# Kernel tuning notes

Measured on AMD Instinct MI355X. Metric: run time of the kernel, lower is better.

Reference implementation:

```python
import jax
import jax.numpy as jnp
from jax import lax
import numpy as np

VOCAB = 50000
EMB = 32
HID = 32
LAYERS = 4
BATCH = 8192
SEQ = 111


def setup_inputs() -> dict:
    key = jax.random.key(0)
    ks = jax.random.split(key, 12)
    s = 0.1
    x = jax.random.randint(ks[0], (BATCH, SEQ), 0, VOCAB, dtype=jnp.int64 if jax.config.read('jax_enable_x64') else jnp.int32)
    emb = jax.random.normal(ks[1], (VOCAB, EMB), jnp.float32) * s
    # stacked per-layer LSTM weights; layer-0 input dim == EMB == HID so stacking is valid
    Wih = jax.random.normal(ks[2], (LAYERS, 4 * HID, EMB), jnp.float32) * s
    Whh = jax.random.normal(ks[3], (LAYERS, 4 * HID, HID), jnp.float32) * s
    bih = jax.random.normal(ks[4], (LAYERS, 4 * HID), jnp.float32) * s
    bhh = jax.random.normal(ks[5], (LAYERS, 4 * HID), jnp.float32) * s
    Wa = jax.random.normal(ks[6], (HID, 1), jnp.float32) * s
    ba = jax.random.normal(ks[7], (1,), jnp.float32) * s
    W1 = jax.random.normal(ks[8], (HID, 32), jnp.float32) * s
    b1 = jax.random.normal(ks[9], (32,), jnp.float32) * s
    W2 = jax.random.normal(ks[10], (32, 3), jnp.float32) * s
    b2 = jax.random.normal(ks[11], (3,), jnp.float32) * s
    return {"x": x, "emb": emb, "Wih": Wih, "Whh": Whh, "bih": bih, "bhh": bhh,
            "Wa": Wa, "ba": ba, "W1": W1, "b1": b1, "W2": W2, "b2": b2}


def _lstm_layer(x, Wih, Whh, bih, bhh):
    # x: [B, T, D] -> [B, T, H]; PyTorch gate order: i, f, g, o
    B = x.shape[0]
    H = Whh.shape[1]
    # precompute the input contribution for all timesteps (one big GEMM)
    xg = jnp.einsum('btd,gd->btg', x, Wih) + bih + bhh  # [B, T, 4H]

    def step(carry, xg_t):
        h, c = carry
        z = xg_t + h @ Whh.T  # [B, 4H]
        i, f, g, o = jnp.split(z, 4, axis=-1)
        c = jax.nn.sigmoid(f) * c + jax.nn.sigmoid(i) * jnp.tanh(g)
        h = jax.nn.sigmoid(o) * jnp.tanh(c)
        return (h, c), h

    init = (jnp.zeros((B, H), x.dtype), jnp.zeros((B, H), x.dtype))
    _, hs = lax.scan(step, init, jnp.swapaxes(xg, 0, 1))  # hs: [T, B, H]
    return jnp.swapaxes(hs, 0, 1)


def reference(x, emb, Wih, Whh, bih, bhh, Wa, ba, W1, b1, W2, b2):
    h = emb[x]  # [B, T, E]
    for l in range(Wih.shape[0]):  # fixed 4 layers
        h = _lstm_layer(h, Wih[l], Whh[l], bih[l], bhh[l])
    scores = h @ Wa + ba                       # [B, T, 1]
    attn = jax.nn.softmax(scores, axis=1)      # softmax over time
    context = jnp.sum(h * attn, axis=1)        # [B, H]
    hid = jnp.tanh(context @ W1 + b1)          # dropout is identity at eval
    return hid @ W2 + b2                       # [B, 3]
```

## Files before the change

### kernel.cpp

```cpp
#include <hip/hip_runtime.h>

#define TSEQ 111
#define L2E 1.44269504088896340736f
#define TWO_L2E 2.88539008177792680472f

using f32x4  = __attribute__((ext_vector_type(4))) float;
using f32x2  = __attribute__((ext_vector_type(2))) float;
using short8 = __attribute__((ext_vector_type(8))) short;

union FragU { unsigned u[4]; uint4 v; short8 s; };

__device__ __forceinline__ float fexp2(float x) { return __builtin_amdgcn_exp2f(x); }
__device__ __forceinline__ float frcp(float x)  { return __builtin_amdgcn_rcpf(x); }
__device__ __forceinline__ float tanh2(float zs) { return 1.f - 2.f * frcp(1.f + fexp2(zs + zs)); }
__device__ __forceinline__ f32x2 exp2v(f32x2 x) { f32x2 r; r[0] = fexp2(x[0]); r[1] = fexp2(x[1]); return r; }
__device__ __forceinline__ f32x2 rcpv(f32x2 x)  { f32x2 r; r[0] = frcp(x[0]); r[1] = frcp(x[1]); return r; }

__device__ __forceinline__ unsigned rnd_bf16(float w) {
  unsigned u = __float_as_uint(w);
  return (u + 0x7fffu + ((u >> 16) & 1u)) >> 16;
}
__device__ __forceinline__ unsigned cvtpk(float a, float b) {
  unsigned r;
  asm("v_cvt_pk_bf16_f32 %0, %1, %2" : "=v"(r) : "v"(a), "v"(b));
  return r;
}

__global__ __launch_bounds__(512, 4) void lstm_fused(
    const int* __restrict__ x, const float* __restrict__ emb,
    const float* __restrict__ Wih, const float* __restrict__ Whh,
    const float* __restrict__ bih, const float* __restrict__ bhh,
    const float* __restrict__ Wa, const float* __restrict__ W1,
    const float* __restrict__ b1, const float* __restrict__ W2,
    const float* __restrict__ b2, float* __restrict__ out)
{
  __shared__ __align__(16) unsigned short hb[2 * 4 * 512];

  const int tid  = threadIdx.x;
  const int wvu  = __builtin_amdgcn_readfirstlane(tid) >> 6;
  const int l    = wvu >> 1;
  const int hf   = wvu & 1;
  const int lane = tid & 63;
  const int c    = lane & 15;
  const int q    = lane >> 4;
  const int gcc  = (c & 3) ^ (c >> 2);
  const int rowbase = blockIdx.x * 16;
  const int xrow = (rowbase + c) * TSEQ;

  const int rdOff = c * 32 + ((q ^ gcc) << 3);
  const int wrOff = c * 32 + ((((2 * hf + (q >> 1)) ^ gcc) << 3) | ((q & 1) << 2));

  FragU wihf[4], whhf[4];
#pragma unroll
  for (int g = 0; g < 4; ++g) {
    const float sj = (g == 2) ? TWO_L2E : -L2E;
    const int wr = 32 * g + 16 * hf + c;
    const float* srcI = Wih + l * 4096 + wr * 32 + 8 * q;
    const float* srcH = Whh + l * 4096 + wr * 32 + 8 * q;
#pragma unroll
    for (int p = 0; p < 4; ++p) {
      wihf[g].u[p] = rnd_bf16(srcI[2 * p] * sj) | (rnd_bf16(srcI[2 * p + 1] * sj) << 16);
      whhf[g].u[p] = rnd_bf16(srcH[2 * p] * sj) | (rnd_bf16(srcH[2 * p + 1] * sj) << 16);
    }
  }
  f32x4 bvv[4];
#pragma unroll
  for (int g = 0; g < 4; ++g) {
    const float sj = (g == 2) ? TWO_L2E : -L2E;
    const int bi = l * 128 + 32 * g + 16 * hf + 4 * q;
#pragma unroll
    for (int e = 0; e < 4; ++e)
      bvv[g][e] = (bih[bi + e] + bhh[bi + e]) * sj;
  }

  FragU wahA, walA;
#pragma unroll
  for (int p = 0; p < 4; ++p) { wahA.u[p] = 0u; walA.u[p] = 0u; }
  if (l == 3) {
#pragma unroll
    for (int p = 0; p < 4; ++p) {
      const int k0 = 8 * q + 2 * p;
      float w0 = Wa[k0] * L2E, w1 = Wa[k0 + 1] * L2E;
      unsigned h0 = rnd_bf16(w0), h1b = rnd_bf16(w1);
      wahA.u[p] = h0 | (h1b << 16);
      float l0v = w0 - __uint_as_float(h0 << 16);
      float l1v = w1 - __uint_as_float(h1b << 16);
      walA.u[p] = rnd_bf16(l0v) | (rnd_bf16(l1v) << 16);
    }
  }

  f32x2 cs2[2];
  cs2[0] = (f32x2){0.f, 0.f}; cs2[1] = (f32x2){0.f, 0.f};
  float mr = -1e30f, sr = 0.f, cx[4];
#pragma unroll
  for (int e = 0; e < 4; ++e) cx[e] = 0.f;

  for (int i = tid; i < 2 * 4 * 512 / 2; i += 512) ((unsigned*)hb)[i] = 0u;

  float4 emA = make_float4(0.f, 0.f, 0.f, 0.f), emB = emA;
  int idxn = 0;
  if (l == 0) {
    int i0 = x[xrow];
    emA = *(const float4*)(emb + i0 * 32 + 8 * q);
    emB = *(const float4*)(emb + i0 * 32 + 8 * q + 4);
    idxn = x[xrow + 1];
  }
  __syncthreads();

#pragma unroll 2
  for (int s = 0; s < TSEQ + 4; ++s) {
    const int t = s - l;
    const bool active = ((unsigned)t < (unsigned)TSEQ);
    const int rp = (s + 1) & 1;
    const int wp = s & 1;
    const bool doAtt = (l == 3) && (s >= 4);

    FragU fi, fh;
    __builtin_amdgcn_s_setprio(1);
    if (active) {
      if (l == 0) {
        fi.u[0] = cvtpk(emA.x, emA.y); fi.u[1] = cvtpk(emA.z, emA.w);
        fi.u[2] = cvtpk(emB.x, emB.y); fi.u[3] = cvtpk(emB.z, emB.w);
        if (t + 1 < TSEQ) {
          emA = *(const float4*)(emb + idxn * 32 + 8 * q);
          emB = *(const float4*)(emb + idxn * 32 + 8 * q + 4);
        }
        if (t + 2 < TSEQ) idxn = x[xrow + t + 2];
      } else {
        fi.v = *(const uint4*)(hb + (rp * 4 + (l - 1)) * 512 + rdOff);
      }
    }
    if (active || doAtt)
      fh.v = *(const uint4*)(hb + (rp * 4 + l) * 512 + rdOff);

    f32x4 acc[4];
    if (active) {
#pragma unroll
      for (int g = 0; g < 4; ++g) {
        acc[g] = __builtin_amdgcn_mfma_f32_16x16x32_bf16(wihf[g].s, fi.s, bvv[g], 0, 0, 0);
        acc[g] = __builtin_amdgcn_mfma_f32_16x16x32_bf16(whhf[g].s, fh.s, acc[g], 0, 0, 0);
      }
    }
    f32x4 sacc;
    if (doAtt) {
      f32x4 z = {0.f, 0.f, 0.f, 0.f};
      sacc = __builtin_amdgcn_mfma_f32_16x16x32_bf16(wahA.s, fh.s, z, 0, 0, 0);
      sacc = __builtin_amdgcn_mfma_f32_16x16x32_bf16(walA.s, fh.s, sacc, 0, 0, 0);
    }
    __builtin_amdgcn_s_setprio(0);

    if (active) {
      float hv[4];
      const f32x2 one = {1.f, 1.f};
      const f32x2 tl2 = {TWO_L2E, TWO_L2E};
#pragma unroll
      for (int pr2 = 0; pr2 < 2; ++pr2) {
        const int e0 = 2 * pr2;
        f32x2 va; va[0] = acc[0][e0]; va[1] = acc[0][e0 + 1];
        f32x2 vm; vm[0] = acc[1][e0]; vm[1] = acc[1][e0 + 1];
        f32x2 vb; vb[0] = acc[2][e0]; vb[1] = acc[2][e0 + 1];
        f32x2 vp; vp[0] = acc[3][e0]; vp[1] = acc[3][e0 + 1];
        f32x2 ea = exp2v(va), em_ = exp2v(vm), eb = exp2v(vb), ep = exp2v(vp);
        f32x2 P  = (one + ea) * (one + eb);
        f32x2 M1 = one + em_;
        f32x2 num = cs2[pr2] * P + (eb - one) * M1;
        f32x2 cn = num * rcpv(M1 * P);
        cs2[pr2] = cn;
        f32x2 qa = cn * tl2;
        qa[0] = fminf(qa[0], 80.f); qa[1] = fminf(qa[1], 80.f);
        f32x2 qv = exp2v(qa);
        f32x2 hvv = (qv - one) * rcpv((one + ep) * (one + qv));
        hv[e0] = hvv[0]; hv[e0 + 1] = hvv[1];
      }

      *(uint2*)(hb + (wp * 4 + l) * 512 + wrOff) =
          make_uint2(cvtpk(hv[0], hv[1]), cvtpk(hv[2], hv[3]));
    }

    if (doAtt) {
      float pf = sacc[0];
      float mn = fmaxf(mr, pf);
      float sc = fexp2(mr - mn);
      float pr = fexp2(pf - mn);
      sr = sr * sc + pr;
#pragma unroll
      for (int p = 0; p < 2; ++p) {
        unsigned w = fh.u[2 * hf + p];
        float vlo = __uint_as_float(w << 16);
        float vhi = __uint_as_float(w & 0xffff0000u);
        cx[2 * p]     = cx[2 * p]     * sc + pr * vlo;
        cx[2 * p + 1] = cx[2 * p + 1] * sc + pr * vhi;
      }
      mr = mn;
    }

    asm volatile("s_waitcnt lgkmcnt(0)\n\ts_barrier" ::: "memory");
  }

  __syncthreads();

  float* cb = (float*)hb;
  if (l == 3) {
    float inv = frcp(sr);
#pragma unroll
    for (int e = 0; e < 4; ++e)
      cb[c * 33 + 8 * q + 4 * hf + e] = cx[e] * inv;
  }
  __syncthreads();
  if (wvu != 6) return;

  float a0[4], a1[4];
  {
    float bb0 = b1[c], bb1 = b1[c + 16];
#pragma unroll
    for (int e = 0; e < 4; ++e) { a0[e] = bb0; a1[e] = bb1; }
    for (int j = 0; j < 32; ++j) {
      float w0 = W1[j * 32 + c];
      float w1 = W1[j * 32 + c + 16];
#pragma unroll
      for (int e = 0; e < 4; ++e) {
        float cr = cb[(4 * q + e) * 33 + j];
        a0[e] = fmaf(cr, w0, a0[e]);
        a1[e] = fmaf(cr, w1, a1[e]);
      }
    }
  }
  float o0[4], o1[4], o2[4];
  {
    float w20 = W2[c * 3 + 0], w21 = W2[c * 3 + 1], w22 = W2[c * 3 + 2];
    float w30 = W2[(c + 16) * 3 + 0], w31 = W2[(c + 16) * 3 + 1], w32 = W2[(c + 16) * 3 + 2];
#pragma unroll
    for (int e = 0; e < 4; ++e) {
      float h0 = tanh2(a0[e] * L2E);
      float hB = tanh2(a1[e] * L2E);
      o0[e] = h0 * w20 + hB * w30;
      o1[e] = h0 * w21 + hB * w31;
      o2[e] = h0 * w22 + hB * w32;
    }
  }
#pragma unroll
  for (int mk = 1; mk <= 8; mk <<= 1) {
#pragma unroll
    for (int e = 0; e < 4; ++e) {
      o0[e] += __shfl_xor(o0[e], mk, 64);
      o1[e] += __shfl_xor(o1[e], mk, 64);
      o2[e] += __shfl_xor(o2[e], mk, 64);
    }
  }
  if (c < 3) {
    float bb = b2[c];
#pragma unroll
    for (int e = 0; e < 4; ++e) {
      float v = (c == 0) ? o0[e] : ((c == 1) ? o1[e] : o2[e]);
      out[(rowbase + 4 * q + e) * 3 + c] = v + bb;
    }
  }
}

extern "C" void kernel_launch(void* const* d_in, const int* in_sizes, int n_in,
                              void* d_out, int out_size, void* d_ws, size_t ws_size,
                              hipStream_t stream) {
  const int*   x   = (const int*)d_in[0];
  const float* emb = (const float*)d_in[1];
  const float* Wih = (const float*)d_in[2];
  const float* Whh = (const float*)d_in[3];
  const float* bih = (const float*)d_in[4];
  const float* bhh = (const float*)d_in[5];
  const float* Wa  = (const float*)d_in[6];
  const float* W1  = (const float*)d_in[8];
  const float* b1  = (const float*)d_in[9];
  const float* W2  = (const float*)d_in[10];
  const float* b2  = (const float*)d_in[11];
  float* out = (float*)d_out;

  lstm_fused<<<512, 512, 0, stream>>>(x, emb, Wih, Whh, bih, bhh, Wa, W1, b1, W2, b2, out);
}
```

Baseline: 159.8 us.

## Process two 16-row batch tiles per block to interleave independent recurrences

Each block now handles 32 batch rows as two independent 16-row tiles, so every wave issues two sets of MFMAs and gate computations per timestep. The grid is halved and shared memory doubled to hold both tiles' hidden states. The intent is to give each wave independent work to hide MFMA and transcendental latency along the serial recurrence and to amortize the per-step barrier. The cost is higher register pressure (launch bounds relaxed to 2) and fewer blocks overall.

```diff
diff --git a/kernel.cpp b/kernel.cpp
--- a/kernel.cpp
+++ b/kernel.cpp
@@ -26,7 +26,31 @@
   return r;
 }
 
-__global__ __launch_bounds__(512, 4) void lstm_fused(
+__device__ __forceinline__ void gates(const f32x4 acc[4], f32x2 cs2[2], float hv[4]) {
+  const f32x2 one = {1.f, 1.f};
+  const f32x2 tl2 = {TWO_L2E, TWO_L2E};
+#pragma unroll
+  for (int pr2 = 0; pr2 < 2; ++pr2) {
+    const int e0 = 2 * pr2;
+    f32x2 va; va[0] = acc[0][e0]; va[1] = acc[0][e0 + 1];
+    f32x2 vm; vm[0] = acc[1][e0]; vm[1] = acc[1][e0 + 1];
+    f32x2 vb; vb[0] = acc[2][e0]; vb[1] = acc[2][e0 + 1];
+    f32x2 vp; vp[0] = acc[3][e0]; vp[1] = acc[3][e0 + 1];
+    f32x2 ea = exp2v(va), em_ = exp2v(vm), eb = exp2v(vb), ep = exp2v(vp);
+    f32x2 P  = (one + ea) * (one + eb);
+    f32x2 M1 = one + em_;
+    f32x2 num = cs2[pr2] * P + (eb - one) * M1;
+    f32x2 cn = num * rcpv(M1 * P);
+    cs2[pr2] = cn;
+    f32x2 qa = cn * tl2;
+    qa[0] = fminf(qa[0], 80.f); qa[1] = fminf(qa[1], 80.f);
+    f32x2 qv = exp2v(qa);
+    f32x2 hvv = (qv - one) * rcpv((one + ep) * (one + qv));
+    hv[e0] = hvv[0]; hv[e0 + 1] = hvv[1];
+  }
+}
+
+__global__ __launch_bounds__(512, 2) void lstm_fused(
     const int* __restrict__ x, const float* __restrict__ emb,
     const float* __restrict__ Wih, const float* __restrict__ Whh,
     const float* __restrict__ bih, const float* __restrict__ bhh,
@@ -34,7 +58,7 @@
     const float* __restrict__ b1, const float* __restrict__ W2,
     const float* __restrict__ b2, float* __restrict__ out)
 {
-  __shared__ __align__(16) unsigned short hb[2 * 4 * 512];
+  __shared__ __align__(16) unsigned short hb[2 * 4 * 1024];
 
   const int tid  = threadIdx.x;
   const int wvu  = __builtin_amdgcn_readfirstlane(tid) >> 6;
@@ -44,8 +68,9 @@
   const int c    = lane & 15;
   const int q    = lane >> 4;
   const int gcc  = (c & 3) ^ (c >> 2);
-  const int rowbase = blockIdx.x * 16;
-  const int xrow = (rowbase + c) * TSEQ;
+  const int rowbase = blockIdx.x * 32;
+  const int xrow0 = (rowbase + c) * TSEQ;
+  const int xrow1 = (rowbase + 16 + c) * TSEQ;
 
   const int rdOff = c * 32 + ((q ^ gcc) << 3);
   const int wrOff = c * 32 + ((((2 * hf + (q >> 1)) ^ gcc) << 3) | ((q & 1) << 2));
@@ -89,21 +114,27 @@
     }
   }
 
-  f32x2 cs2[2];
-  cs2[0] = (f32x2){0.f, 0.f}; cs2[1] = (f32x2){0.f, 0.f};
-  float mr = -1e30f, sr = 0.f, cx[4];
-#pragma unroll
-  for (int e = 0; e < 4; ++e) cx[e] = 0.f;
-
-  for (int i = tid; i < 2 * 4 * 512 / 2; i += 512) ((unsigned*)hb)[i] = 0u;
-
-  float4 emA = make_float4(0.f, 0.f, 0.f, 0.f), emB = emA;
-  int idxn = 0;
+  f32x2 csA[2], csB[2];
+  csA[0] = (f32x2){0.f, 0.f}; csA[1] = (f32x2){0.f, 0.f};
+  csB[0] = (f32x2){0.f, 0.f}; csB[1] = (f32x2){0.f, 0.f};
+  float mr0 = -1e30f, sr0 = 0.f, cx0[4];
+  float mr1 = -1e30f, sr1 = 0.f, cx1[4];
+#pragma unroll
+  for (int e = 0; e < 4; ++e) { cx0[e] = 0.f; cx1[e] = 0.f; }
+
+  for (int i = tid; i < 2 * 4 * 1024 / 2; i += 512) ((unsigned*)hb)[i] = 0u;
+
+  float4 emA0 = make_float4(0.f, 0.f, 0.f, 0.f), emB0 = emA0, emA1 = emA0, emB1 = emA0;
+  int idxn0 = 0, idxn1 = 0;
   if (l == 0) {
-    int i0 = x[xrow];
-    emA = *(const float4*)(emb + i0 * 32 + 8 * q);
-    emB = *(const float4*)(emb + i0 * 32 + 8 * q + 4);
-    idxn = x[xrow + 1];
+    int i00 = x[xrow0];
+    emA0 = *(const float4*)(emb + i00 * 32 + 8 * q);
+    emB0 = *(const float4*)(emb + i00 * 32 + 8 * q + 4);
+    int i01 = x[xrow1];
+    emA1 = *(const float4*)(emb + i01 * 32 + 8 * q);
+    emB1 = *(const float4*)(emb + i01 * 32 + 8 * q + 4);
+    idxn0 = x[xrow0 + 1];
+    idxn1 = x[xrow1 + 1];
   }
   __syncthreads();
 
@@ -115,83 +146,93 @@
     const int wp = s & 1;
     const bool doAtt = (l == 3) && (s >= 4);
 
-    FragU fi, fh;
+    FragU fi0, fh0, fi1, fh1;
     __builtin_amdgcn_s_setprio(1);
     if (active) {
       if (l == 0) {
-        fi.u[0] = cvtpk(emA.x, emA.y); fi.u[1] = cvtpk(emA.z, emA.w);
-        fi.u[2] = cvtpk(emB.x, emB.y); fi.u[3] = cvtpk(emB.z, emB.w);
+        fi0.u[0] = cvtpk(emA0.x, emA0.y); fi0.u[1] = cvtpk(emA0.z, emA0.w);
+        fi0.u[2] = cvtpk(emB0.x, emB0.y); fi0.u[3] = cvtpk(emB0.z, emB0.w);
+        fi1.u[0] = cvtpk(emA1.x, emA1.y); fi1.u[1] = cvtpk(emA1.z, emA1.w);
+        fi1.u[2] = cvtpk(emB1.x, emB1.y); fi1.u[3] = cvtpk(emB1.z, emB1.w);
         if (t + 1 < TSEQ) {
-          emA = *(const float4*)(emb + idxn * 32 + 8 * q);
-          emB = *(const float4*)(emb + idxn * 32 + 8 * q + 4);
+          emA0 = *(const float4*)(emb + idxn0 * 32 + 8 * q);
+          emB0 = *(const float4*)(emb + idxn0 * 32 + 8 * q + 4);
+          emA1 = *(const float4*)(emb + idxn1 * 32 + 8 * q);
+          emB1 = *(const float4*)(emb + idxn1 * 32 + 8 * q + 4);
         }
-        if (t + 2 < TSEQ) idxn = x[xrow + t + 2];
+        if (t + 2 < TSEQ) { idxn0 = x[xrow0 + t + 2]; idxn1 = x[xrow1 + t + 2]; }
       } else {
-        fi.v = *(const uint4*)(hb + (rp * 4 + (l - 1)) * 512 + rdOff);
-      }
-    }
-    if (active || doAtt)
-      fh.v = *(const uint4*)(hb + (rp * 4 + l) * 512 + rdOff);
-
-    f32x4 acc[4];
+        fi0.v = *(const uint4*)(hb + (rp * 4 + (l - 1)) * 1024 + rdOff);
+        fi1.v = *(const uint4*)(hb + (rp * 4 + (l - 1)) * 1024 + rdOff + 512);
+      }
+    }
+    if (active || doAtt) {
+      fh0.v = *(const uint4*)(hb + (rp * 4 + l) * 1024 + rdOff);
+      fh1.v = *(const uint4*)(hb + (rp * 4 + l) * 1024 + rdOff + 512);
+    }
+
+    f32x4 acc0[4], acc1[4];
     if (active) {
 #pragma unroll
       for (int g = 0; g < 4; ++g) {
-        acc[g] = __builtin_amdgcn_mfma_f32_16x16x32_bf16(wihf[g].s, fi.s, bvv[g], 0, 0, 0);
-        acc[g] = __builtin_amdgcn_mfma_f32_16x16x32_bf16(whhf[g].s, fh.s, acc[g], 0, 0, 0);
-      }
-    }
-    f32x4 sacc;
+        acc0[g] = __builtin_amdgcn_mfma_f32_16x16x32_bf16(wihf[g].s, fi0.s, bvv[g], 0, 0, 0);
+        acc0[g] = __builtin_amdgcn_mfma_f32_16x16x32_bf16(whhf[g].s, fh0.s, acc0[g], 0, 0, 0);
+      }
+#pragma unroll
+      for (int g = 0; g < 4; ++g) {
+        acc1[g] = __builtin_amdgcn_mfma_f32_16x16x32_bf16(wihf[g].s, fi1.s, bvv[g], 0, 0, 0);
+        acc1[g] = __builtin_amdgcn_mfma_f32_16x16x32_bf16(whhf[g].s, fh1.s, acc1[g], 0, 0, 0);
+      }
+    }
+    f32x4 sacc0, sacc1;
     if (doAtt) {
       f32x4 z = {0.f, 0.f, 0.f, 0.f};
-      sacc = __builtin_amdgcn_mfma_f32_16x16x32_bf16(wahA.s, fh.s, z, 0, 0, 0);
-      sacc = __builtin_amdgcn_mfma_f32_16x16x32_bf16(walA.s, fh.s, sacc, 0, 0, 0);
+      sacc0 = __builtin_amdgcn_mfma_f32_16x16x32_bf16(wahA.s, fh0.s, z, 0, 0, 0);
+      sacc0 = __builtin_amdgcn_mfma_f32_16x16x32_bf16(walA.s, fh0.s, sacc0, 0, 0, 0);
+      sacc1 = __builtin_amdgcn_mfma_f32_16x16x32_bf16(wahA.s, fh1.s, z, 0, 0, 0);
+      sacc1 = __builtin_amdgcn_mfma_f32_16x16x32_bf16(walA.s, fh1.s, sacc1, 0, 0, 0);
     }
     __builtin_amdgcn_s_setprio(0);
 
     if (active) {
-      float hv[4];
-      const f32x2 one = {1.f, 1.f};
-      const f32x2 tl2 = {TWO_L2E, TWO_L2E};
-#pragma unroll
-      for (int pr2 = 0; pr2 < 2; ++pr2) {
-        const int e0 = 2 * pr2;
-        f32x2 va; va[0] = acc[0][e0]; va[1] = acc[0][e0 + 1];
-        f32x2 vm; vm[0] = acc[1][e0]; vm[1] = acc[1][e0 + 1];
-        f32x2 vb; vb[0] = acc[2][e0]; vb[1] = acc[2][e0 + 1];
-        f32x2 vp; vp[0] = acc[3][e0]; vp[1] = acc[3][e0 + 1];
-        f32x2 ea = exp2v(va), em_ = exp2v(vm), eb = exp2v(vb), ep = exp2v(vp);
-        f32x2 P  = (one + ea) * (one + eb);
-        f32x2 M1 = one + em_;
-        f32x2 num = cs2[pr2] * P + (eb - one) * M1;
-        f32x2 cn = num * rcpv(M1 * P);
-        cs2[pr2] = cn;
-        f32x2 qa = cn * tl2;
-        qa[0] = fminf(qa[0], 80.f); qa[1] = fminf(qa[1], 80.f);
-        f32x2 qv = exp2v(qa);
-        f32x2 hvv = (qv - one) * rcpv((one + ep) * (one + qv));
-        hv[e0] = hvv[0]; hv[e0 + 1] = hvv[1];
-      }
-
-      *(uint2*)(hb + (wp * 4 + l) * 512 + wrOff) =
-          make_uint2(cvtpk(hv[0], hv[1]), cvtpk(hv[2], hv[3]));
+      float hv0[4], hv1[4];
+      gates(acc0, csA, hv0);
+      *(uint2*)(hb + (wp * 4 + l) * 1024 + wrOff) =
+          make_uint2(cvtpk(hv0[0], hv0[1]), cvtpk(hv0[2], hv0[3]));
+      gates(acc1, csB, hv1);
+      *(uint2*)(hb + (wp * 4 + l) * 1024 + wrOff + 512) =
+          make_uint2(cvtpk(hv1[0], hv1[1]), cvtpk(hv1[2], hv1[3]));
     }
 
     if (doAtt) {
-      float pf = sacc[0];
-      float mn = fmaxf(mr, pf);
-      float sc = fexp2(mr - mn);
-      float pr = fexp2(pf - mn);
-      sr = sr * sc + pr;
-#pragma unroll
-      for (int p = 0; p < 2; ++p) {
-        unsigned w = fh.u[2 * hf + p];
-        float vlo = __uint_as_float(w << 16);
-        float vhi = __uint_as_float(w & 0xffff0000u);
-        cx[2 * p]     = cx[2 * p]     * sc + pr * vlo;
-        cx[2 * p + 1] = cx[2 * p + 1] * sc + pr * vhi;
-      }
-      mr = mn;
+      {
+        float pf = sacc0[0];
+        float mn = fmaxf(mr0, pf);
+        float sc = fexp2(mr0 - mn);
+        float pr = fexp2(pf - mn);
+        sr0 = sr0 * sc + pr;
+#pragma unroll
+        for (int p = 0; p < 2; ++p) {
+          unsigned w = fh0.u[2 * hf + p];
+          cx0[2 * p]     = cx0[2 * p]     * sc + pr * __uint_as_float(w << 16);
+          cx0[2 * p + 1] = cx0[2 * p + 1] * sc + pr * __uint_as_float(w & 0xffff0000u);
+        }
+        mr0 = mn;
+      }
+      {
+        float pf = sacc1[0];
+        float mn = fmaxf(mr1, pf);
+        float sc = fexp2(mr1 - mn);
+        float pr = fexp2(pf - mn);
+        sr1 = sr1 * sc + pr;
+#pragma unroll
+        for (int p = 0; p < 2; ++p) {
+          unsigned w = fh1.u[2 * hf + p];
+          cx1[2 * p]     = cx1[2 * p]     * sc + pr * __uint_as_float(w << 16);
+          cx1[2 * p + 1] = cx1[2 * p + 1] * sc + pr * __uint_as_float(w & 0xffff0000u);
+        }
+        mr1 = mn;
+      }
     }
 
     asm volatile("s_waitcnt lgkmcnt(0)\n\ts_barrier" ::: "memory");
@@ -201,13 +242,16 @@
 
   float* cb = (float*)hb;
   if (l == 3) {
-    float inv = frcp(sr);
-#pragma unroll
-    for (int e = 0; e < 4; ++e)
-      cb[c * 33 + 8 * q + 4 * hf + e] = cx[e] * inv;
+    float inv0 = frcp(sr0), inv1 = frcp(sr1);
+#pragma unroll
+    for (int e = 0; e < 4; ++e) {
+      cb[c * 33 + 8 * q + 4 * hf + e]        = cx0[e] * inv0;
+      cb[(16 + c) * 33 + 8 * q + 4 * hf + e] = cx1[e] * inv1;
+    }
   }
   __syncthreads();
-  if (wvu != 6) return;
+  if (wvu != 6 && wvu != 7) return;
+  const int rb2 = (wvu - 6) * 16;
 
   float a0[4], a1[4];
   {
@@ -219,7 +263,7 @@
       float w1 = W1[j * 32 + c + 16];
 #pragma unroll
       for (int e = 0; e < 4; ++e) {
-        float cr = cb[(4 * q + e) * 33 + j];
+        float cr = cb[(rb2 + 4 * q + e) * 33 + j];
         a0[e] = fmaf(cr, w0, a0[e]);
         a1[e] = fmaf(cr, w1, a1[e]);
       }
@@ -252,7 +296,7 @@
 #pragma unroll
     for (int e = 0; e < 4; ++e) {
       float v = (c == 0) ? o0[e] : ((c == 1) ? o1[e] : o2[e]);
-      out[(rowbase + 4 * q + e) * 3 + c] = v + bb;
+      out[(rowbase + rb2 + 4 * q + e) * 3 + c] = v + bb;
     }
   }
 }
@@ -273,5 +317,5 @@
   const float* b2  = (const float*)d_in[11];
   float* out = (float*)d_out;
 
-  lstm_fused<<<512, 512, 0, stream>>>(x, emb, Wih, Whh, bih, bhh, Wa, W1, b1, W2, b2, out);
-}
+  lstm_fused<<<256, 512, 0, stream>>>(x, emb, Wih, Whh, bih, bhh, Wa, W1, b1, W2, b2, out);
+}
```

New measurement: 169.3 us. +6.0%, slower.
